# Optimization experiments

Hardware: AMD Instinct MI355X
Metric: run time of the kernel (lower is better)

The kernel has to match this reference:

```python
import jax, jax.numpy as jnp
import numpy as np

# Dimensions: T time steps, B sequences, F input features, H hidden width, S=1 state size
T, B, F = 4096, 128, 1
H = 256
S = 1
DT = 1.0  # init kwarg dt


def setup_inputs() -> dict:
    key = jax.random.key(0)
    k = jax.random.split(key, 4)
    return {
        "x": jax.random.normal(k[0], (T, B, F), jnp.float32),
        # derivative-network MLP params: input = concat(state, input sample)
        "W1": jax.random.normal(k[1], (S + F, H), jnp.float32) * (1.0 / np.sqrt(S + F)),
        "b1": jnp.zeros((H,), jnp.float32),
        "W2": jax.random.normal(k[2], (H, H), jnp.float32) * (1.0 / np.sqrt(H)),
        "b2": jnp.zeros((H,), jnp.float32),
        "W3": jax.random.normal(k[3], (H, S), jnp.float32) * (1.0 / np.sqrt(H)),
        "b3": jnp.zeros((S,), jnp.float32),
    }


def reference(x, W1, b1, W2, b2, W3, b3):
    """Forward-Euler ODE integration over the time axis of x.

    x: (T, B, F). Returns trajectory of the scalar state, shape (T, B, 1),
    where traj[0] is the zero initial state (odeint returns values at the
    requested time points, starting with the initial value).
    """
    Bsz = x.shape[1]
    y0 = jnp.zeros((Bsz, S), x.dtype)

    def mlp(y, xt):  # derivative network f(t, y): (B,S),(B,F) -> (B,S)
        inp = jnp.concatenate([y, xt], axis=-1)          # (B, S+F)
        h = jnp.tanh(inp @ W1 + b1)                      # (B, H)
        h = jnp.tanh(h @ W2 + b2)                        # (B, H)
        return h @ W3 + b3                               # (B, S)

    def step(y, xt):
        y_next = y + DT * mlp(y, xt)                     # forward Euler
        return y_next, y                                 # emit state at t_n

    _, traj = jax.lax.scan(step, y0, x)                  # traj: (T, B, S)
    return traj
```

## Files before the change

kernel.cpp:

```cpp
#include <hip/hip_runtime.h>

#define T_STEPS 4096
#define BATCH   128
#define HID     256

typedef float f4 __attribute__((ext_vector_type(4)));

__device__ __forceinline__ float fast_tanh(float z) {
    float e = __expf(2.0f * z);
    return 1.0f - 2.0f / (e + 1.0f);
}

#define RPT32(M) M(0) M(1) M(2) M(3) M(4) M(5) M(6) M(7) \
                 M(8) M(9) M(10) M(11) M(12) M(13) M(14) M(15) \
                 M(16) M(17) M(18) M(19) M(20) M(21) M(22) M(23) \
                 M(24) M(25) M(26) M(27) M(28) M(29) M(30) M(31)

__global__ __launch_bounds__(512, 2)
void odenet_kernel(const float* __restrict__ x,
                   const float* __restrict__ W1, const float* __restrict__ b1,
                   const float* __restrict__ W2, const float* __restrict__ b2,
                   const float* __restrict__ W3, const float* __restrict__ b3,
                   float* __restrict__ out)
{
    const int b = blockIdx.x;
    const int t = threadIdx.x;
    const int w = t >> 6;
    const int l = t & 63;

    __shared__ float x_lds[T_STEPS];
    __shared__ float h1_lds[HID];
    __shared__ float part[8][HID];
    __shared__ __align__(16) float red[4];

    for (int i = t; i < T_STEPS; i += 512) x_lds[i] = x[i * BATCH + b];

    #define DECLQ(i) \
        f4 wq##i = *(const f4*)(W2 + (32*w + (i)) * HID + 4*l); \
        asm volatile("" : "+v"(wq##i));
    RPT32(DECLQ)

    const int  j   = t & 255;
    const float w1a = W1[j];
    const float w1b = W1[HID + j];
    const float b1v = b1[j];
    const float b2v = b2[j];
    const float w3v = W3[j];
    const float b3v = b3[0];

    float y = 0.0f;
    __syncthreads();

    #pragma unroll 1
    for (int n = 0; n < T_STEPS; ++n) {
        if (t == 256) out[n * BATCH + b] = y;
        if (t < 256) {
            float xt = x_lds[n];
            h1_lds[t] = fast_tanh(fmaf(y, w1a, fmaf(xt, w1b, b1v)));
        }
        __syncthreads();

        f4 acc = {0.f, 0.f, 0.f, 0.f};
        const f4* h4 = ((const f4*)h1_lds) + 8 * w;
        #define GQUAD(g, q0, q1, q2, q3) { \
            f4 hq = h4[g]; \
            acc += hq.x * wq##q0; \
            acc += hq.y * wq##q1; \
            acc += hq.z * wq##q2; \
            acc += hq.w * wq##q3; }
        GQUAD(0,  0,  1,  2,  3)
        GQUAD(1,  4,  5,  6,  7)
        GQUAD(2,  8,  9, 10, 11)
        GQUAD(3, 12, 13, 14, 15)
        GQUAD(4, 16, 17, 18, 19)
        GQUAD(5, 20, 21, 22, 23)
        GQUAD(6, 24, 25, 26, 27)
        GQUAD(7, 28, 29, 30, 31)

        *(f4*)(&part[w][4 * l]) = acc;
        __syncthreads();

        if (t < 256) {
            float s = ((part[0][t] + part[1][t]) + (part[2][t] + part[3][t]))
                    + ((part[4][t] + part[5][t]) + (part[6][t] + part[7][t]))
                    + b2v;
            float h2 = fast_tanh(s);
            float p  = h2 * w3v;
            #pragma unroll
            for (int m = 32; m >= 1; m >>= 1) p += __shfl_xor(p, m, 64);
            if (l == 0) red[w] = p;
        }
        __syncthreads();

        f4 r = *(const f4*)red;
        y += ((r.x + r.y) + (r.z + r.w)) + b3v;
    }
}

extern "C" void kernel_launch(void* const* d_in, const int* in_sizes, int n_in,
                              void* d_out, int out_size, void* d_ws, size_t ws_size,
                              hipStream_t stream) {
    const float* x  = (const float*)d_in[0];
    const float* W1 = (const float*)d_in[1];
    const float* b1 = (const float*)d_in[2];
    const float* W2 = (const float*)d_in[3];
    const float* b2 = (const float*)d_in[4];
    const float* W3 = (const float*)d_in[5];
    const float* b3 = (const float*)d_in[6];
    float* out = (float*)d_out;

    odenet_kernel<<<dim3(BATCH), dim3(512), 0, stream>>>(x, W1, b1, W2, b2, W3, b3, out);
}
```

Before: 4.213 ms.

## Use 1024 threads with readlane broadcast of h1 and DPP reduction

Doubles the block to 1024 threads so each wave holds 16 rows of W2 in registers instead of 32. Every wave now computes its own 16 layer-1 activations redundantly and broadcasts them with readlane, which removes the h1 shared-memory round trip and one barrier per step. The final dot-product reduction uses DPP row shifts and broadcasts in place of shfl_xor. The costs are 16-way partial sums, twice as many waves taking part in each barrier, and 16 serial readlane operations per step.

```diff
diff --git a/kernel.cpp b/kernel.cpp
--- a/kernel.cpp
+++ b/kernel.cpp
@@ -11,12 +11,20 @@
     return 1.0f - 2.0f / (e + 1.0f);
 }
 
-#define RPT32(M) M(0) M(1) M(2) M(3) M(4) M(5) M(6) M(7) \
-                 M(8) M(9) M(10) M(11) M(12) M(13) M(14) M(15) \
-                 M(16) M(17) M(18) M(19) M(20) M(21) M(22) M(23) \
-                 M(24) M(25) M(26) M(27) M(28) M(29) M(30) M(31)
+__device__ __forceinline__ float rlane(float v, int l) {
+    return __uint_as_float(__builtin_amdgcn_readlane(__float_as_uint(v), l));
+}
 
-__global__ __launch_bounds__(512, 2)
+template <int CTRL, int ROW_MASK>
+__device__ __forceinline__ float dpp_add(float x) {
+    int s = __builtin_amdgcn_update_dpp(0, __float_as_int(x), CTRL, ROW_MASK, 0xf, false);
+    return x + __int_as_float(s);
+}
+
+#define RPT16(M) M(0) M(1) M(2) M(3) M(4) M(5) M(6) M(7) \
+                 M(8) M(9) M(10) M(11) M(12) M(13) M(14) M(15)
+
+__global__ __launch_bounds__(1024, 4)
 void odenet_kernel(const float* __restrict__ x,
                    const float* __restrict__ W1, const float* __restrict__ b1,
                    const float* __restrict__ W2, const float* __restrict__ b2,
@@ -27,25 +35,25 @@
     const int t = threadIdx.x;
     const int w = t >> 6;
     const int l = t & 63;
+    const int k = 16 * w + (l & 15);
 
     __shared__ float x_lds[T_STEPS];
-    __shared__ float h1_lds[HID];
-    __shared__ float part[8][HID];
+    __shared__ float part[16][HID];
     __shared__ __align__(16) float red[4];
 
-    for (int i = t; i < T_STEPS; i += 512) x_lds[i] = x[i * BATCH + b];
+    for (int i = t; i < T_STEPS; i += 1024) x_lds[i] = x[i * BATCH + b];
 
     #define DECLQ(i) \
-        f4 wq##i = *(const f4*)(W2 + (32*w + (i)) * HID + 4*l); \
+        f4 wq##i = *(const f4*)(W2 + (16*w + (i)) * HID + 4*l); \
         asm volatile("" : "+v"(wq##i));
-    RPT32(DECLQ)
+    RPT16(DECLQ)
 
-    const int  j   = t & 255;
-    const float w1a = W1[j];
-    const float w1b = W1[HID + j];
-    const float b1v = b1[j];
-    const float b2v = b2[j];
-    const float w3v = W3[j];
+    const float w1a = W1[k];
+    const float w1b = W1[HID + k];
+    const float b1v = b1[k];
+
+    const float b2v = (t < 256) ? b2[t] : 0.f;
+    const float w3v = (t < 256) ? W3[t] : 0.f;
     const float b3v = b3[0];
 
     float y = 0.0f;
@@ -53,42 +61,35 @@
 
     #pragma unroll 1
     for (int n = 0; n < T_STEPS; ++n) {
-        if (t == 256) out[n * BATCH + b] = y;
-        if (t < 256) {
-            float xt = x_lds[n];
-            h1_lds[t] = fast_tanh(fmaf(y, w1a, fmaf(xt, w1b, b1v)));
-        }
-        __syncthreads();
+        if (t == 1023) out[n * BATCH + b] = y;
+
+        const float xt = x_lds[n];
+        const float h  = fast_tanh(fmaf(y, w1a, fmaf(xt, w1b, b1v)));
 
         f4 acc = {0.f, 0.f, 0.f, 0.f};
-        const f4* h4 = ((const f4*)h1_lds) + 8 * w;
-        #define GQUAD(g, q0, q1, q2, q3) { \
-            f4 hq = h4[g]; \
-            acc += hq.x * wq##q0; \
-            acc += hq.y * wq##q1; \
-            acc += hq.z * wq##q2; \
-            acc += hq.w * wq##q3; }
-        GQUAD(0,  0,  1,  2,  3)
-        GQUAD(1,  4,  5,  6,  7)
-        GQUAD(2,  8,  9, 10, 11)
-        GQUAD(3, 12, 13, 14, 15)
-        GQUAD(4, 16, 17, 18, 19)
-        GQUAD(5, 20, 21, 22, 23)
-        GQUAD(6, 24, 25, 26, 27)
-        GQUAD(7, 28, 29, 30, 31)
-
+        #define STEPK(i) { const float s = rlane(h, i); acc += s * wq##i; }
+        RPT16(STEPK)
         *(f4*)(&part[w][4 * l]) = acc;
         __syncthreads();
 
         if (t < 256) {
-            float s = ((part[0][t] + part[1][t]) + (part[2][t] + part[3][t]))
-                    + ((part[4][t] + part[5][t]) + (part[6][t] + part[7][t]))
-                    + b2v;
-            float h2 = fast_tanh(s);
+            float s0 = 0.f, s1 = 0.f, s2 = 0.f, s3 = 0.f;
+            #pragma unroll
+            for (int p = 0; p < 4; ++p) {
+                s0 += part[4*p + 0][t];
+                s1 += part[4*p + 1][t];
+                s2 += part[4*p + 2][t];
+                s3 += part[4*p + 3][t];
+            }
+            float h2 = fast_tanh(((s0 + s1) + (s2 + s3)) + b2v);
             float p  = h2 * w3v;
-            #pragma unroll
-            for (int m = 32; m >= 1; m >>= 1) p += __shfl_xor(p, m, 64);
-            if (l == 0) red[w] = p;
+            p = dpp_add<0x111, 0xf>(p);
+            p = dpp_add<0x112, 0xf>(p);
+            p = dpp_add<0x114, 0xf>(p);
+            p = dpp_add<0x118, 0xf>(p);
+            p = dpp_add<0x142, 0xa>(p);
+            p = dpp_add<0x143, 0xc>(p);
+            if (l == 63) red[w] = p;
         }
         __syncthreads();
 
@@ -109,5 +110,5 @@
     const float* b3 = (const float*)d_in[6];
     float* out = (float*)d_out;
 
-    odenet_kernel<<<dim3(BATCH), dim3(512), 0, stream>>>(x, W1, b1, W2, b2, W3, b3, out);
+    odenet_kernel<<<dim3(BATCH), dim3(1024), 0, stream>>>(x, W1, b1, W2, b2, W3, b3, out);
 }
```

Measured after the change: 3.577 ms. 1.18x faster.
